# Performance work log

Hardware: AMD Instinct MI355X
Metric: run time of the kernel (lower is better)

## Reference

```python
import jax, jax.numpy as jnp
import numpy as np

N, IN_F, OUT_F = 8192, 512, 256
ALPHA = 0.2  # LeakyReLU negative slope
NEG_INF = -9e15


def setup_inputs() -> dict:
    key = jax.random.key(0)
    k1, k2, k3, k4 = jax.random.split(key, 4)
    input = jax.random.normal(k1, (N, IN_F), dtype=jnp.float32)
    adj = jax.random.randint(k2, (N, N), 0, 2, dtype=jnp.int32)
    # Xavier-like scale for params
    W = jax.random.normal(k3, (IN_F, OUT_F), dtype=jnp.float32) * (1.414 * np.sqrt(2.0 / (IN_F + OUT_F)))
    a = jax.random.normal(k4, (2 * OUT_F, 1), dtype=jnp.float32) * (1.414 * np.sqrt(2.0 / (2 * OUT_F + 1)))
    return {"input": input, "adj": adj, "W": W, "a": a}


def reference(input, adj, W, a):
    h = input @ W                                   # [N, F]
    a1, a2 = a[:OUT_F, 0], a[OUT_F:, 0]             # [F], [F]
    # e[i, j] = leakyrelu(h_i . a1 + h_j . a2) -- equivalent to concat+linear
    s1 = h @ a1                                     # [N]
    s2 = h @ a2                                     # [N]
    e = jax.nn.leaky_relu(s1[:, None] + s2[None, :], negative_slope=ALPHA)  # [N, N]
    e = jnp.where(adj > 0, e, NEG_INF)
    attention = jax.nn.softmax(e, axis=1)           # row-wise softmax
    # dropout p=0.0 / eval mode -> identity
    h_prime = attention @ h                          # [N, F]
    return jax.nn.elu(h_prime)                       # concat=True -> elu
```

## Files before the change

### kernel.cpp

```cpp
#include <hip/hip_runtime.h>
#include <stdint.h>

#define N_NODES 8192
#define IN_FEAT 512
#define OUT_FEAT 256
#define LOG2E 1.4426950408889634f

typedef __bf16 b16x8 __attribute__((ext_vector_type(8)));
typedef unsigned short u16x8v __attribute__((ext_vector_type(8)));
typedef float f32x4 __attribute__((ext_vector_type(4)));

static __device__ __forceinline__ unsigned short f2bf(float f) {
    union { float f; uint32_t u; } v; v.f = f;
    uint32_t r = v.u + 0x7FFFu + ((v.u >> 16) & 1u);
    return (unsigned short)(r >> 16);
}

__global__ __launch_bounds__(256) void k0_transpose_w(const float* __restrict__ W,
                                                      unsigned short* __restrict__ Wt) {
    int tid = blockIdx.x * 256 + threadIdx.x;
    int c = tid & (OUT_FEAT - 1);
    int k = tid >> 8;
    Wt[(size_t)c * IN_FEAT + k] = f2bf(W[(size_t)k * OUT_FEAT + c]);
}

__global__ __launch_bounds__(256) void k1_hgemm(const float* __restrict__ input,
                                                const unsigned short* __restrict__ Wt,
                                                const float* __restrict__ a_vec,
                                                unsigned short* __restrict__ hTf,
                                                float* __restrict__ s1_raw,
                                                float* __restrict__ s2_raw) {
    int tid = threadIdx.x;
    int lane = tid & 63;
    int c = lane & 15, g = lane >> 4;
    int r0 = blockIdx.x * 64 + (tid >> 6) * 16;
    f32x4 acc[16];
#pragma unroll
    for (int t = 0; t < 16; ++t) acc[t] = (f32x4){0.f, 0.f, 0.f, 0.f};
    const float* arow = input + (size_t)(r0 + c) * IN_FEAT;
#pragma unroll 1
    for (int kk = 0; kk < IN_FEAT / 32; ++kk) {
        int kb = kk * 32 + 8 * g;
        float4 x0 = *(const float4*)(arow + kb);
        float4 x1 = *(const float4*)(arow + kb + 4);
        u16x8v au;
        au[0] = f2bf(x0.x); au[1] = f2bf(x0.y); au[2] = f2bf(x0.z); au[3] = f2bf(x0.w);
        au[4] = f2bf(x1.x); au[5] = f2bf(x1.y); au[6] = f2bf(x1.z); au[7] = f2bf(x1.w);
        b16x8 af = __builtin_bit_cast(b16x8, au);
#pragma unroll
        for (int t = 0; t < 16; ++t) {
            b16x8 bf = __builtin_bit_cast(b16x8,
                *(const u16x8v*)(Wt + (size_t)(16 * t + c) * IN_FEAT + kb));
            acc[t] = __builtin_amdgcn_mfma_f32_16x16x32_bf16(af, bf, acc[t], 0, 0, 0);
        }
    }
    float a1v[16], a2v[16];
#pragma unroll
    for (int t = 0; t < 16; ++t) {
        a1v[t] = a_vec[16 * t + c];
        a2v[t] = a_vec[OUT_FEAT + 16 * t + c];
    }
#pragma unroll
    for (int r = 0; r < 4; ++r) {
        float s1p = 0.f, s2p = 0.f;
#pragma unroll
        for (int t = 0; t < 16; ++t) { s1p += acc[t][r] * a1v[t]; s2p += acc[t][r] * a2v[t]; }
#pragma unroll
        for (int m = 1; m <= 8; m <<= 1) { s1p += __shfl_xor(s1p, m); s2p += __shfl_xor(s2p, m); }
        if (c == 0) {
            int row = r0 + 4 * g + r;
            s1_raw[row] = s1p;
            s2_raw[row] = s2p;
        }
    }
    int chunk = r0 >> 5;
    int lp = ((r0 & 16) >> 3) + (g >> 1);
    int e0 = 4 * (g & 1);
#pragma unroll
    for (int t = 0; t < 16; ++t) {
        ushort4 pk;
        pk.x = f2bf(acc[t][0]); pk.y = f2bf(acc[t][1]);
        pk.z = f2bf(acc[t][2]); pk.w = f2bf(acc[t][3]);
        *(ushort4*)(hTf + ((size_t)(chunk * 16 + t) * 64 + lp * 16 + c) * 8 + e0) = pk;
    }
}

__global__ __launch_bounds__(256) void k2_prep(const float* __restrict__ s1_raw,
                                               const float* __restrict__ s2_raw,
                                               float* __restrict__ s2k,
                                               float2* __restrict__ row2) {
    __shared__ float red[256];
    int tid = threadIdx.x;
    float m = -3.0e38f;
    for (int j = tid; j < N_NODES; j += 256) m = fmaxf(m, s2_raw[j]);
    red[tid] = m;
    __syncthreads();
    for (int s = 128; s > 0; s >>= 1) {
        if (tid < s) red[tid] = fmaxf(red[tid], red[tid + s]);
        __syncthreads();
    }
    float M2 = red[0];
    int i = blockIdx.x * 256 + tid;
    float s1 = s1_raw[i];
    float u = s1 + M2;
    float mi = fmaxf(u, 0.2f * u);
    row2[i] = make_float2((s1 - mi) * LOG2E, -0.8f * mi * LOG2E);
    s2k[i] = s2_raw[i] * LOG2E;
}

__global__ __launch_bounds__(256, 3) void k3_flash(const int* __restrict__ adj,
                                                   const unsigned short* __restrict__ hTf,
                                                   const float* __restrict__ s2k,
                                                   const float2* __restrict__ row2,
                                                   float* __restrict__ pout,
                                                   float* __restrict__ rowpart) {
    __shared__ __align__(16) unsigned short tiles[2][8192];
    __shared__ uint32_t lmaskD[2][64];
    __shared__ __align__(16) float ls2k[2048];

    int tid = threadIdx.x;
    int w = tid >> 6, lane = tid & 63;
    int c = lane & 15, g = lane >> 4;
    int ch = w & 1, rq = w >> 1;
    int jq = blockIdx.x & 3;
    int rg = blockIdx.x >> 2;
    int rowbase = rg * 64 + rq * 32;

    int mrow = tid >> 2;
    int mg8 = tid & 3;
    const int* adjbase = adj + (size_t)(rg * 64 + mrow) * N_NODES + jq * 2048 + mg8 * 8;

    *(float4*)&ls2k[tid * 8]     = *(const float4*)(s2k + jq * 2048 + tid * 8);
    *(float4*)&ls2k[tid * 8 + 4] = *(const float4*)(s2k + jq * 2048 + tid * 8 + 4);
    {
        int4 v0 = *(const int4*)(adjbase);
        int4 v1 = *(const int4*)(adjbase + 4);
        unsigned b = (unsigned)(v0.x != 0) | ((unsigned)(v0.y != 0) << 1)
                   | ((unsigned)(v0.z != 0) << 2) | ((unsigned)(v0.w != 0) << 3)
                   | ((unsigned)(v1.x != 0) << 4) | ((unsigned)(v1.y != 0) << 5)
                   | ((unsigned)(v1.z != 0) << 6) | ((unsigned)(v1.w != 0) << 7);
        ((unsigned char*)&lmaskD[0][mrow])[mg8] = (unsigned char)b;
    }
    __builtin_amdgcn_sched_barrier(0);
    {
        int jc = jq * 64;
#pragma unroll
        for (int q = 0; q < 4; ++q) {
            int ti = w * 4 + q;
            const unsigned short* src = hTf + (size_t)jc * 8192 + (size_t)(ti * 64 + lane) * 8;
            __builtin_amdgcn_global_load_lds(
                (const __attribute__((address_space(1))) uint32_t*)src,
                (__attribute__((address_space(3))) uint32_t*)(&tiles[0][ti * 512]), 16, 0, 0);
        }
    }
    __builtin_amdgcn_sched_barrier(0);
    int4 va0 = *(const int4*)(adjbase + 32);
    int4 va1 = *(const int4*)(adjbase + 36);
    __builtin_amdgcn_sched_barrier(0);
    asm volatile("s_waitcnt vmcnt(2) lgkmcnt(0)" ::: "memory");
    __builtin_amdgcn_sched_barrier(0);
    __builtin_amdgcn_s_barrier();
    __builtin_amdgcn_sched_barrier(0);

    float2 rc0 = row2[rowbase + c];
    float2 rc1 = row2[rowbase + 16 + c];
    float a_row0 = rc0.x, m8_0 = rc0.y;
    float a_row1 = rc1.x, m8_1 = rc1.y;

    f32x4 acc0[8], acc1[8];
#pragma unroll
    for (int t = 0; t < 8; ++t) { acc0[t] = (f32x4){0,0,0,0}; acc1[t] = (f32x4){0,0,0,0}; }
    float lacc0 = 0.f, lacc1 = 0.f;

#define SCORE_AND_MFMA(CUR, KK)                                                          \
    {                                                                                    \
        uint32_t md0 = lmaskD[CUR][rq * 32 + c];                                         \
        uint32_t md1 = lmaskD[CUR][rq * 32 + 16 + c];                                    \
        uint32_t mb0 = (md0 >> (8 * g)) & 0xFFu;                                         \
        uint32_t mb1 = (md1 >> (8 * g)) & 0xFFu;                                         \
        const float* sp = &ls2k[(KK) * 32 + 8 * g];                                      \
        float4 s0 = *(const float4*)sp;                                                  \
        float4 s1v = *(const float4*)(sp + 4);                                           \
        float sv[8] = {s0.x, s0.y, s0.z, s0.w, s1v.x, s1v.y, s1v.z, s1v.w};              \
        b16x8 af0, af1;                                                                  \
        _Pragma("unroll")                                                                \
        for (int e = 0; e < 8; ++e) {                                                    \
            float va = a_row0 + sv[e];                                                   \
            float vb = __builtin_fmaf(va, 0.2f, m8_0);                                   \
            float p0 = (mb0 & (1u << e)) ? __builtin_amdgcn_exp2f(fmaxf(va, vb)) : 0.f;  \
            lacc0 += p0;                                                                 \
            af0[e] = (__bf16)p0;                                                         \
            float vc = a_row1 + sv[e];                                                   \
            float vd = __builtin_fmaf(vc, 0.2f, m8_1);                                   \
            float p1 = (mb1 & (1u << e)) ? __builtin_amdgcn_exp2f(fmaxf(vc, vd)) : 0.f;  \
            lacc1 += p1;                                                                 \
            af1[e] = (__bf16)p1;                                                         \
        }                                                                                \
        const unsigned short* tb = &tiles[CUR][ch * 8 * 512];                            \
        _Pragma("unroll")                                                                \
        for (int t = 0; t < 8; ++t) {                                                    \
            b16x8 bf = __builtin_bit_cast(b16x8, *(const u16x8v*)(tb + t * 512 + lane * 8)); \
            acc0[t] = __builtin_amdgcn_mfma_f32_16x16x32_bf16(af0, bf, acc0[t], 0, 0, 0); \
            acc1[t] = __builtin_amdgcn_mfma_f32_16x16x32_bf16(af1, bf, acc1[t], 0, 0, 0); \
        }                                                                                \
    }

#define PACK_NEXT(CURX)                                                                  \
    {                                                                                    \
        unsigned b = (unsigned)(va0.x != 0) | ((unsigned)(va0.y != 0) << 1)              \
                   | ((unsigned)(va0.z != 0) << 2) | ((unsigned)(va0.w != 0) << 3)       \
                   | ((unsigned)(va1.x != 0) << 4) | ((unsigned)(va1.y != 0) << 5)       \
                   | ((unsigned)(va1.z != 0) << 6) | ((unsigned)(va1.w != 0) << 7);      \
        ((unsigned char*)&lmaskD[(CURX) ^ 1][mrow])[mg8] = (unsigned char)b;             \
    }

#pragma unroll 2
    for (int kk = 0; kk < 62; ++kk) {
        int cur = kk & 1;
        {
            int jc = jq * 64 + kk + 1;
#pragma unroll
            for (int q = 0; q < 4; ++q) {
                int ti = w * 4 + q;
                const unsigned short* src = hTf + (size_t)jc * 8192 + (size_t)(ti * 64 + lane) * 8;
                __builtin_amdgcn_global_load_lds(
                    (const __attribute__((address_space(1))) uint32_t*)src,
                    (__attribute__((address_space(3))) uint32_t*)(&tiles[cur ^ 1][ti * 512]), 16, 0, 0);
            }
        }
        __builtin_amdgcn_sched_barrier(0);
        int4 vb0 = *(const int4*)(adjbase + (kk + 2) * 32);
        int4 vb1 = *(const int4*)(adjbase + (kk + 2) * 32 + 4);
        __builtin_amdgcn_sched_barrier(0);
        SCORE_AND_MFMA(cur, kk)
        PACK_NEXT(cur)
        va0 = vb0; va1 = vb1;
        __builtin_amdgcn_sched_barrier(0);
        asm volatile("s_waitcnt vmcnt(2) lgkmcnt(0)" ::: "memory");
        __builtin_amdgcn_sched_barrier(0);
        __builtin_amdgcn_s_barrier();
        __builtin_amdgcn_sched_barrier(0);
    }
    {
        int jc = jq * 64 + 63;
#pragma unroll
        for (int q = 0; q < 4; ++q) {
            int ti = w * 4 + q;
            const unsigned short* src = hTf + (size_t)jc * 8192 + (size_t)(ti * 64 + lane) * 8;
            __builtin_amdgcn_global_load_lds(
                (const __attribute__((address_space(1))) uint32_t*)src,
                (__attribute__((address_space(3))) uint32_t*)(&tiles[1][ti * 512]), 16, 0, 0);
        }
        __builtin_amdgcn_sched_barrier(0);
        SCORE_AND_MFMA(0, 62)
        PACK_NEXT(0)
        __builtin_amdgcn_sched_barrier(0);
        asm volatile("s_waitcnt vmcnt(0) lgkmcnt(0)" ::: "memory");
        __builtin_amdgcn_sched_barrier(0);
        __builtin_amdgcn_s_barrier();
        __builtin_amdgcn_sched_barrier(0);
    }
    SCORE_AND_MFMA(1, 63)

    float l0 = lacc0 + __shfl_xor(lacc0, 16); l0 += __shfl_xor(l0, 32);
    float l1 = lacc1 + __shfl_xor(lacc1, 16); l1 += __shfl_xor(l1, 32);
    if (ch == 0 && g == 0) {
        rowpart[jq * N_NODES + rowbase + c] = l0;
        rowpart[jq * N_NODES + rowbase + 16 + c] = l1;
    }

#pragma unroll
    for (int r = 0; r < 4; ++r) {
        int grow0 = rowbase + 4 * g + r;
        int grow1 = grow0 + 16;
#pragma unroll
        for (int t = 0; t < 8; ++t) {
            pout[((size_t)jq * N_NODES + grow0) * OUT_FEAT + ch * 128 + 16 * t + c] = acc0[t][r];
            pout[((size_t)jq * N_NODES + grow1) * OUT_FEAT + ch * 128 + 16 * t + c] = acc1[t][r];
        }
    }
#undef SCORE_AND_MFMA
#undef PACK_NEXT
}

__global__ __launch_bounds__(256) void k4_reduce(const float* __restrict__ pout,
                                                 const float* __restrict__ rowpart,
                                                 float* __restrict__ out) {
    int t = blockIdx.x * 256 + threadIdx.x;
    int row = t >> 8;
    float s = 0.f, l = 0.f;
#pragma unroll
    for (int q = 0; q < 4; ++q) {
        s += pout[(size_t)q * N_NODES * OUT_FEAT + t];
        l += rowpart[q * N_NODES + row];
    }
    float inv = (l > 0.f) ? 1.0f / l : 0.f;
    float x = s * inv;
    out[t] = (x > 0.f) ? x : (__builtin_amdgcn_exp2f(x * LOG2E) - 1.0f);
}

extern "C" void kernel_launch(void* const* d_in, const int* in_sizes, int n_in,
                              void* d_out, int out_size, void* d_ws, size_t ws_size,
                              hipStream_t stream) {
    const float* input = (const float*)d_in[0];
    const int* adj = (const int*)d_in[1];
    const float* W = (const float*)d_in[2];
    const float* a_vec = (const float*)d_in[3];
    float* out = (float*)d_out;

    char* ws = (char*)d_ws;
    unsigned short* Wt  = (unsigned short*)(ws);
    unsigned short* hTf = (unsigned short*)(ws + 262144);
    float*  s2k     = (float*)(ws + 4456448);
    float2* row2    = (float2*)(ws + 4489216);
    float*  s1_raw  = (float*)(ws + 4554752);
    float*  s2_raw  = (float*)(ws + 4587520);
    float*  rowpart = (float*)(ws + 13008896);
    float*  pout    = (float*)(ws + 13139968);

    hipLaunchKernelGGL(k0_transpose_w, dim3(512), dim3(256), 0, stream, W, Wt);
    hipLaunchKernelGGL(k1_hgemm, dim3(N_NODES / 64), dim3(256), 0, stream,
                       input, Wt, a_vec, hTf, s1_raw, s2_raw);
    hipLaunchKernelGGL(k2_prep, dim3(32), dim3(256), 0, stream, s1_raw, s2_raw, s2k, row2);
    hipLaunchKernelGGL(k3_flash, dim3(512), dim3(256), 0, stream,
                       adj, hTf, s2k, row2, pout, rowpart);
    hipLaunchKernelGGL(k4_reduce, dim3(N_NODES * OUT_FEAT / 256), dim3(256), 0, stream,
                       pout, rowpart, out);
}
```

Before: 168.4 us.

## Factor exp of leaky-relu scores into per-row/col products and triple-buffer tiles

The attention weight exp(leakyrelu(s1+s2)-m) is rewritten as max(E1_i*e1_j, E2_i*e2_j), with the exponentials precomputed per row and per column in the prep kernel. This removes the per-element exp2 from the inner flash loop and replaces it with two multiplies and a max. The hT tile and adjacency mask pipeline also moves from double to triple buffering with a prefetch depth of two, and occupancy drops from 3 to 2 blocks per SM to make room for the extra LDS. The risks are possible float underflow or overflow in the separated exponentials and lower occupancy.

```diff
diff --git a/kernel.cpp b/kernel.cpp
--- a/kernel.cpp
+++ b/kernel.cpp
@@ -87,7 +87,7 @@
 
 __global__ __launch_bounds__(256) void k2_prep(const float* __restrict__ s1_raw,
                                                const float* __restrict__ s2_raw,
-                                               float* __restrict__ s2k,
+                                               float* __restrict__ e12,
                                                float2* __restrict__ row2) {
     __shared__ float red[256];
     int tid = threadIdx.x;
@@ -104,19 +104,22 @@
     float s1 = s1_raw[i];
     float u = s1 + M2;
     float mi = fmaxf(u, 0.2f * u);
-    row2[i] = make_float2((s1 - mi) * LOG2E, -0.8f * mi * LOG2E);
-    s2k[i] = s2_raw[i] * LOG2E;
-}
-
-__global__ __launch_bounds__(256, 3) void k3_flash(const int* __restrict__ adj,
+    row2[i] = make_float2(__builtin_amdgcn_exp2f((s1 - mi) * LOG2E),
+                          __builtin_amdgcn_exp2f((0.2f * s1 - mi) * LOG2E));
+    float s2 = s2_raw[i];
+    e12[2 * i]     = __builtin_amdgcn_exp2f(s2 * LOG2E);
+    e12[2 * i + 1] = __builtin_amdgcn_exp2f(0.2f * s2 * LOG2E);
+}
+
+__global__ __launch_bounds__(256, 2) void k3_flash(const int* __restrict__ adj,
                                                    const unsigned short* __restrict__ hTf,
-                                                   const float* __restrict__ s2k,
+                                                   const float* __restrict__ e12g,
                                                    const float2* __restrict__ row2,
                                                    float* __restrict__ pout,
                                                    float* __restrict__ rowpart) {
-    __shared__ __align__(16) unsigned short tiles[2][8192];
-    __shared__ uint32_t lmaskD[2][64];
-    __shared__ __align__(16) float ls2k[2048];
+    __shared__ __align__(16) unsigned short tiles[3][8192];
+    __shared__ uint32_t lmaskD[3][64];
+    __shared__ __align__(16) float le12[4096];
 
     int tid = threadIdx.x;
     int w = tid >> 6, lane = tid & 63;
@@ -130,42 +133,54 @@
     int mg8 = tid & 3;
     const int* adjbase = adj + (size_t)(rg * 64 + mrow) * N_NODES + jq * 2048 + mg8 * 8;
 
-    *(float4*)&ls2k[tid * 8]     = *(const float4*)(s2k + jq * 2048 + tid * 8);
-    *(float4*)&ls2k[tid * 8 + 4] = *(const float4*)(s2k + jq * 2048 + tid * 8 + 4);
+#define PACK_TO(BUF, V0, V1)                                                             \
+    {                                                                                    \
+        unsigned b = (unsigned)((V0).x != 0) | ((unsigned)((V0).y != 0) << 1)            \
+                   | ((unsigned)((V0).z != 0) << 2) | ((unsigned)((V0).w != 0) << 3)     \
+                   | ((unsigned)((V1).x != 0) << 4) | ((unsigned)((V1).y != 0) << 5)     \
+                   | ((unsigned)((V1).z != 0) << 6) | ((unsigned)((V1).w != 0) << 7);    \
+        ((unsigned char*)&lmaskD[BUF][mrow])[mg8] = (unsigned char)b;                    \
+    }
+
+    float2 rc0 = row2[rowbase + c];
+    float2 rc1 = row2[rowbase + 16 + c];
+    float E1r0 = rc0.x, E2r0 = rc0.y;
+    float E1r1 = rc1.x, E2r1 = rc1.y;
+#pragma unroll
+    for (int q = 0; q < 4; ++q) {
+        *(float4*)&le12[tid * 16 + q * 4] =
+            *(const float4*)(e12g + (size_t)jq * 4096 + tid * 16 + q * 4);
+    }
     {
         int4 v0 = *(const int4*)(adjbase);
         int4 v1 = *(const int4*)(adjbase + 4);
-        unsigned b = (unsigned)(v0.x != 0) | ((unsigned)(v0.y != 0) << 1)
-                   | ((unsigned)(v0.z != 0) << 2) | ((unsigned)(v0.w != 0) << 3)
-                   | ((unsigned)(v1.x != 0) << 4) | ((unsigned)(v1.y != 0) << 5)
-                   | ((unsigned)(v1.z != 0) << 6) | ((unsigned)(v1.w != 0) << 7);
-        ((unsigned char*)&lmaskD[0][mrow])[mg8] = (unsigned char)b;
-    }
-    __builtin_amdgcn_sched_barrier(0);
-    {
-        int jc = jq * 64;
+        int4 v2 = *(const int4*)(adjbase + 32);
+        int4 v3 = *(const int4*)(adjbase + 36);
+        PACK_TO(0, v0, v1)
+        PACK_TO(1, v2, v3)
+    }
+    __builtin_amdgcn_sched_barrier(0);
+#pragma unroll
+    for (int b = 0; b < 2; ++b) {
+        size_t jc = (size_t)(jq * 64 + b) * 8192;
 #pragma unroll
         for (int q = 0; q < 4; ++q) {
             int ti = w * 4 + q;
-            const unsigned short* src = hTf + (size_t)jc * 8192 + (size_t)(ti * 64 + lane) * 8;
+            const unsigned short* src = hTf + jc + (size_t)(ti * 64 + lane) * 8;
             __builtin_amdgcn_global_load_lds(
                 (const __attribute__((address_space(1))) uint32_t*)src,
-                (__attribute__((address_space(3))) uint32_t*)(&tiles[0][ti * 512]), 16, 0, 0);
-        }
-    }
-    __builtin_amdgcn_sched_barrier(0);
-    int4 va0 = *(const int4*)(adjbase + 32);
-    int4 va1 = *(const int4*)(adjbase + 36);
-    __builtin_amdgcn_sched_barrier(0);
-    asm volatile("s_waitcnt vmcnt(2) lgkmcnt(0)" ::: "memory");
+                (__attribute__((address_space(3))) uint32_t*)(&tiles[b][ti * 512]), 16, 0, 0);
+        }
+    }
+    __builtin_amdgcn_sched_barrier(0);
+    int4 va0 = *(const int4*)(adjbase + 64);
+    int4 va1 = *(const int4*)(adjbase + 68);
+    __builtin_amdgcn_sched_barrier(0);
+    asm volatile("s_waitcnt vmcnt(2)" ::: "memory");
+    asm volatile("s_waitcnt lgkmcnt(0)" ::: "memory");
     __builtin_amdgcn_sched_barrier(0);
     __builtin_amdgcn_s_barrier();
     __builtin_amdgcn_sched_barrier(0);
-
-    float2 rc0 = row2[rowbase + c];
-    float2 rc1 = row2[rowbase + 16 + c];
-    float a_row0 = rc0.x, m8_0 = rc0.y;
-    float a_row1 = rc1.x, m8_1 = rc1.y;
 
     f32x4 acc0[8], acc1[8];
 #pragma unroll
@@ -178,21 +193,20 @@
         uint32_t md1 = lmaskD[CUR][rq * 32 + 16 + c];                                    \
         uint32_t mb0 = (md0 >> (8 * g)) & 0xFFu;                                         \
         uint32_t mb1 = (md1 >> (8 * g)) & 0xFFu;                                         \
-        const float* sp = &ls2k[(KK) * 32 + 8 * g];                                      \
-        float4 s0 = *(const float4*)sp;                                                  \
-        float4 s1v = *(const float4*)(sp + 4);                                           \
-        float sv[8] = {s0.x, s0.y, s0.z, s0.w, s1v.x, s1v.y, s1v.z, s1v.w};              \
+        float ev[16];                                                                    \
+        _Pragma("unroll")                                                                \
+        for (int q = 0; q < 4; ++q)                                                      \
+            *(f32x4*)&ev[q * 4] = *(const f32x4*)&le12[((KK) * 32 + 8 * g) * 2 + q * 4]; \
         b16x8 af0, af1;                                                                  \
         _Pragma("unroll")                                                                \
         for (int e = 0; e < 8; ++e) {                                                    \
-            float va = a_row0 + sv[e];                                                   \
-            float vb = __builtin_fmaf(va, 0.2f, m8_0);                                   \
-            float p0 = (mb0 & (1u << e)) ? __builtin_amdgcn_exp2f(fmaxf(va, vb)) : 0.f;  \
+            float e1 = ev[2 * e], e2 = ev[2 * e + 1];                                    \
+            float q0 = fmaxf(E1r0 * e1, E2r0 * e2);                                      \
+            float p0 = (mb0 & (1u << e)) ? q0 : 0.f;                                     \
             lacc0 += p0;                                                                 \
             af0[e] = (__bf16)p0;                                                         \
-            float vc = a_row1 + sv[e];                                                   \
-            float vd = __builtin_fmaf(vc, 0.2f, m8_1);                                   \
-            float p1 = (mb1 & (1u << e)) ? __builtin_amdgcn_exp2f(fmaxf(vc, vd)) : 0.f;  \
+            float q1 = fmaxf(E1r1 * e1, E2r1 * e2);                                      \
+            float p1 = (mb1 & (1u << e)) ? q1 : 0.f;                                     \
             lacc1 += p1;                                                                 \
             af1[e] = (__bf16)p1;                                                         \
         }                                                                                \
@@ -205,62 +219,71 @@
         }                                                                                \
     }
 
-#define PACK_NEXT(CURX)                                                                  \
-    {                                                                                    \
-        unsigned b = (unsigned)(va0.x != 0) | ((unsigned)(va0.y != 0) << 1)              \
-                   | ((unsigned)(va0.z != 0) << 2) | ((unsigned)(va0.w != 0) << 3)       \
-                   | ((unsigned)(va1.x != 0) << 4) | ((unsigned)(va1.y != 0) << 5)       \
-                   | ((unsigned)(va1.z != 0) << 6) | ((unsigned)(va1.w != 0) << 7);      \
-        ((unsigned char*)&lmaskD[(CURX) ^ 1][mrow])[mg8] = (unsigned char)b;             \
-    }
-
-#pragma unroll 2
-    for (int kk = 0; kk < 62; ++kk) {
-        int cur = kk & 1;
+    int cur = 0;
+    int nx2 = 2;
+#pragma unroll 1
+    for (int kk = 0; kk < 61; ++kk) {
         {
-            int jc = jq * 64 + kk + 1;
+            size_t jc = (size_t)(jq * 64 + kk + 2) * 8192;
 #pragma unroll
             for (int q = 0; q < 4; ++q) {
                 int ti = w * 4 + q;
-                const unsigned short* src = hTf + (size_t)jc * 8192 + (size_t)(ti * 64 + lane) * 8;
+                const unsigned short* src = hTf + jc + (size_t)(ti * 64 + lane) * 8;
                 __builtin_amdgcn_global_load_lds(
                     (const __attribute__((address_space(1))) uint32_t*)src,
-                    (__attribute__((address_space(3))) uint32_t*)(&tiles[cur ^ 1][ti * 512]), 16, 0, 0);
+                    (__attribute__((address_space(3))) uint32_t*)(&tiles[nx2][ti * 512]), 16, 0, 0);
             }
         }
         __builtin_amdgcn_sched_barrier(0);
-        int4 vb0 = *(const int4*)(adjbase + (kk + 2) * 32);
-        int4 vb1 = *(const int4*)(adjbase + (kk + 2) * 32 + 4);
+        int4 vb0 = *(const int4*)(adjbase + (kk + 3) * 32);
+        int4 vb1 = *(const int4*)(adjbase + (kk + 3) * 32 + 4);
         __builtin_amdgcn_sched_barrier(0);
         SCORE_AND_MFMA(cur, kk)
-        PACK_NEXT(cur)
+        __builtin_amdgcn_sched_barrier(0);
+        asm volatile("s_waitcnt vmcnt(6)" ::: "memory");
+        __builtin_amdgcn_sched_barrier(0);
+        PACK_TO(nx2, va0, va1)
         va0 = vb0; va1 = vb1;
         __builtin_amdgcn_sched_barrier(0);
-        asm volatile("s_waitcnt vmcnt(2) lgkmcnt(0)" ::: "memory");
+        asm volatile("s_waitcnt lgkmcnt(0)" ::: "memory");
         __builtin_amdgcn_sched_barrier(0);
         __builtin_amdgcn_s_barrier();
         __builtin_amdgcn_sched_barrier(0);
+        cur = (cur == 2) ? 0 : cur + 1;
+        nx2 = (nx2 == 2) ? 0 : nx2 + 1;
     }
     {
-        int jc = jq * 64 + 63;
+        size_t jc = (size_t)(jq * 64 + 63) * 8192;
 #pragma unroll
         for (int q = 0; q < 4; ++q) {
             int ti = w * 4 + q;
-            const unsigned short* src = hTf + (size_t)jc * 8192 + (size_t)(ti * 64 + lane) * 8;
+            const unsigned short* src = hTf + jc + (size_t)(ti * 64 + lane) * 8;
             __builtin_amdgcn_global_load_lds(
                 (const __attribute__((address_space(1))) uint32_t*)src,
-                (__attribute__((address_space(3))) uint32_t*)(&tiles[1][ti * 512]), 16, 0, 0);
-        }
-        __builtin_amdgcn_sched_barrier(0);
-        SCORE_AND_MFMA(0, 62)
-        PACK_NEXT(0)
-        __builtin_amdgcn_sched_barrier(0);
-        asm volatile("s_waitcnt vmcnt(0) lgkmcnt(0)" ::: "memory");
+                (__attribute__((address_space(3))) uint32_t*)(&tiles[0][ti * 512]), 16, 0, 0);
+        }
+        __builtin_amdgcn_sched_barrier(0);
+        SCORE_AND_MFMA(1, 61)
+        __builtin_amdgcn_sched_barrier(0);
+        asm volatile("s_waitcnt vmcnt(4)" ::: "memory");
+        __builtin_amdgcn_sched_barrier(0);
+        PACK_TO(0, va0, va1)
+        __builtin_amdgcn_sched_barrier(0);
+        asm volatile("s_waitcnt lgkmcnt(0)" ::: "memory");
         __builtin_amdgcn_sched_barrier(0);
         __builtin_amdgcn_s_barrier();
         __builtin_amdgcn_sched_barrier(0);
     }
-    SCORE_AND_MFMA(1, 63)
+    {
+        SCORE_AND_MFMA(2, 62)
+        __builtin_amdgcn_sched_barrier(0);
+        asm volatile("s_waitcnt vmcnt(0)" ::: "memory");
+        asm volatile("s_waitcnt lgkmcnt(0)" ::: "memory");
+        __builtin_amdgcn_sched_barrier(0);
+        __builtin_amdgcn_s_barrier();
+        __builtin_amdgcn_sched_barrier(0);
+    }
+    SCORE_AND_MFMA(0, 63)
 
     float l0 = lacc0 + __shfl_xor(lacc0, 16); l0 += __shfl_xor(l0, 32);
     float l1 = lacc1 + __shfl_xor(lacc1, 16); l1 += __shfl_xor(l1, 32);
@@ -280,7 +303,7 @@
         }
     }
 #undef SCORE_AND_MFMA
-#undef PACK_NEXT
+#undef PACK_TO
 }
 
 __global__ __launch_bounds__(256) void k4_reduce(const float* __restrict__ pout,
@@ -311,19 +334,19 @@
     char* ws = (char*)d_ws;
     unsigned short* Wt  = (unsigned short*)(ws);
     unsigned short* hTf = (unsigned short*)(ws + 262144);
-    float*  s2k     = (float*)(ws + 4456448);
-    float2* row2    = (float2*)(ws + 4489216);
-    float*  s1_raw  = (float*)(ws + 4554752);
-    float*  s2_raw  = (float*)(ws + 4587520);
+    float*  e12     = (float*)(ws + 4456448);
+    float2* row2    = (float2*)(ws + 4521984);
+    float*  s1_raw  = (float*)(ws + 4587520);
+    float*  s2_raw  = (float*)(ws + 4620288);
     float*  rowpart = (float*)(ws + 13008896);
     float*  pout    = (float*)(ws + 13139968);
 
     hipLaunchKernelGGL(k0_transpose_w, dim3(512), dim3(256), 0, stream, W, Wt);
     hipLaunchKernelGGL(k1_hgemm, dim3(N_NODES / 64), dim3(256), 0, stream,
                        input, Wt, a_vec, hTf, s1_raw, s2_raw);
-    hipLaunchKernelGGL(k2_prep, dim3(32), dim3(256), 0, stream, s1_raw, s2_raw, s2k, row2);
+    hipLaunchKernelGGL(k2_prep, dim3(32), dim3(256), 0, stream, s1_raw, s2_raw, e12, row2);
     hipLaunchKernelGGL(k3_flash, dim3(512), dim3(256), 0, stream,
-                       adj, hTf, s2k, row2, pout, rowpart);
+                       adj, hTf, e12, row2, pout, rowpart);
     hipLaunchKernelGGL(k4_reduce, dim3(N_NODES * OUT_FEAT / 256), dim3(256), 0, stream,
                        pout, rowpart, out);
 }
```

Result: slower. 176.3 us (+4.7%).
